# Kernel tuning notes

Hardware: AMD Instinct MI355X
Metric: run time of the kernel (lower is better)

The kernel has to match this reference:

```python
import jax, jax.numpy as jnp
import numpy as np

N, M, DIM, HEADS = 32768, 2048, 128, 8
TAU = 0.1


def setup_inputs() -> dict:
    key = jax.random.key(0)
    ks = jax.random.split(key, 7)
    return {
        "x1": jax.random.normal(ks[0], (N, DIM), jnp.float32),
        "k": jax.random.normal(ks[1], (N, DIM), jnp.float32),
        "c": jax.random.normal(ks[2], (M, DIM), jnp.float32),
        "Wq": jax.random.normal(ks[3], (DIM * HEADS, DIM), jnp.float32) * 0.02,
        "bq": jax.random.normal(ks[4], (DIM * HEADS,), jnp.float32) * 0.02,
        "Wd": jax.random.normal(ks[5], (DIM, DIM), jnp.float32) * 0.02,
        "bd": jax.random.normal(ks[6], (DIM,), jnp.float32) * 0.02,
    }


def reference(x1, k, c, Wq, bq, Wd, bd):
    # q and k both go through the same 'query' projection (as in the source)
    q = x1 @ Wq.T + bq                      # [N, dim*H]
    kq = k @ Wq.T + bq                      # [N, dim*H]
    C = jnp.tile(c, (1, HEADS))             # torch.cat([c]*H, dim=1) -> [M, dim*H]
    t = q + kq                              # additive attention 'scores' input
    logits = (t @ C.T) / jnp.sqrt(jnp.asarray(DIM, t.dtype))  # [N, M]
    p = jax.nn.softmax(logits, axis=-1)
    # gumbel_softmax(p, tau=0.1, hard=True): -log(Exp(1)) ~ Gumbel(0,1)
    noise = jax.random.gumbel(jax.random.key(42), p.shape, p.dtype)
    y_soft = jax.nn.softmax((p + noise) / TAU, axis=-1)
    idx = jnp.argmax(y_soft, axis=-1)
    y_hard = jax.nn.one_hot(idx, M, dtype=p.dtype)
    y = y_hard - jax.lax.stop_gradient(y_soft) + y_soft  # straight-through
    # attention_dropout and dropout are rate 0.0 -> identity
    out = y.T @ x1                          # [M, dim]
    return out @ Wd.T + bd                  # dense
```

## Files before the change

### kernel.cpp

```cpp
#include <hip/hip_runtime.h>
#include <stdint.h>
#include <math.h>

#define NROW 32768
#define MCOL 2048
#define KDIM 128
#define NHEAD 8
#define SCALE 0.08838834764831845f
#define STATS_BLOCKS 512
#define SCAN_BLOCKS 1024
#define CAND_MAX 32

typedef __attribute__((ext_vector_type(8))) short short8;
typedef __attribute__((ext_vector_type(4))) float f32x4;

__device__ __forceinline__ uint32_t rotl32(uint32_t x, uint32_t r) {
  return __builtin_amdgcn_alignbit(x, x, 32u - r);
}
__device__ __forceinline__ uint32_t umin3(uint32_t a, uint32_t b, uint32_t c) {
  return min(min(a, b), c);
}

__device__ __forceinline__ uint32_t tf_hash(uint32_t c) {
  const uint32_t K2 = 0x1BD11BDAu ^ 0u ^ 42u;
  uint32_t x0 = 0u, x1 = c + 42u;
#define R4A { x0 += x1; x1 = rotl32(x1,13); x1 ^= x0; \
              x0 += x1; x1 = rotl32(x1,15); x1 ^= x0; \
              x0 += x1; x1 = rotl32(x1,26); x1 ^= x0; \
              x0 += x1; x1 = rotl32(x1, 6); x1 ^= x0; }
#define R4B { x0 += x1; x1 = rotl32(x1,17); x1 ^= x0; \
              x0 += x1; x1 = rotl32(x1,29); x1 ^= x0; \
              x0 += x1; x1 = rotl32(x1,16); x1 ^= x0; \
              x0 += x1; x1 = rotl32(x1,24); x1 ^= x0; }
  R4A x0 += 42u;      x1 += K2 + 1u;
  R4B x0 += K2;       x1 += 2u;
  R4A    x1 += 42u + 3u;
  R4B x0 += 42u;      x1 += K2 + 4u;
  R4A x0 += K2;       x1 += 5u;
#undef R4A
#undef R4B
  return x0 ^ x1;
}

__device__ __forceinline__ float bits_to_u(uint32_t b) {
  uint32_t fb = (b >> 9) | 0x3F800000u;
  float f = __uint_as_float(fb) - 1.0f;
  return (f == 0.0f) ? 1.17549435e-38f : f;
}

__global__ void k_wsum(const float* __restrict__ Wq, const float* __restrict__ bq,
                       float* __restrict__ Wsum, float* __restrict__ bsum) {
  int t = blockIdx.x * 256 + threadIdx.x;
  if (t < KDIM * KDIM) {
    int d = t >> 7, e = t & 127;
    float s = 0.f;
#pragma unroll
    for (int h = 0; h < NHEAD; ++h) s += Wq[(h * KDIM + d) * KDIM + e];
    Wsum[t] = s;
  }
  if (blockIdx.x == 0 && threadIdx.x < KDIM) {
    int d = threadIdx.x;
    float s = 0.f;
#pragma unroll
    for (int h = 0; h < NHEAD; ++h) s += bq[h * KDIM + d];
    bsum[d] = 2.0f * s;
  }
}

__global__ void k_cw(const float* __restrict__ c, const float* __restrict__ Wsum,
                     const float* __restrict__ bsum,
                     float* __restrict__ cw_s, unsigned short* __restrict__ cwB16,
                     float* __restrict__ cb_s) {
  int m = blockIdx.x;
  int e = threadIdx.x;
  __shared__ float crow[KDIM];
  if (e < 32) ((float4*)crow)[e] = ((const float4*)(c + (size_t)m * KDIM))[e];
  __syncthreads();
  float s = 0.f;
#pragma unroll 4
  for (int d = 0; d < KDIM; ++d) s += crow[d] * Wsum[d * KDIM + e];
  float sv = s * SCALE;
  cw_s[(size_t)m * KDIM + e] = sv;
  {
    int t = m >> 4, col = m & 15, ks = e >> 5, grp = (e >> 3) & 3, j = e & 7;
    int lane = grp * 16 + col;
    cwB16[(((size_t)(t * 4 + ks)) * 64 + lane) * 8 + j] =
        (unsigned short)(__float_as_uint(sv) >> 16);
  }
  if (e == 0) {
    float sb = 0.f;
    for (int d = 0; d < KDIM; ++d) sb += bsum[d] * crow[d];
    cb_s[m] = sb * SCALE;
  }
}

__launch_bounds__(256, 4)
__global__ void k_fused(const float* __restrict__ x1, const float* __restrict__ kin,
                        const uint4* __restrict__ cwB, const float* __restrict__ cb_s,
                        float* __restrict__ rowMx, float* __restrict__ rowD,
                        uint2* __restrict__ cand, int* __restrict__ cnts) {
  const int tid = threadIdx.x;
  const int wv = tid >> 6, lane = tid & 63;

  if (blockIdx.x < STATS_BLOCKS) {
    const int R = blockIdx.x * 64 + wv * 16;
    const int rowA = R + (lane & 15);
    const int kbase = (lane >> 4) * 8;

    union { uint32_t u[4]; short8 s; } af[4];
#pragma unroll
    for (int ks = 0; ks < 4; ++ks) {
      const float* xp = x1 + (size_t)rowA * KDIM + ks * 32 + kbase;
      const float* kp = kin + (size_t)rowA * KDIM + ks * 32 + kbase;
      float4 a0 = *(const float4*)xp, a1 = *(const float4*)(xp + 4);
      float4 b0 = *(const float4*)kp, b1 = *(const float4*)(kp + 4);
      float f[8] = {a0.x + b0.x, a0.y + b0.y, a0.z + b0.z, a0.w + b0.w,
                    a1.x + b1.x, a1.y + b1.y, a1.z + b1.z, a1.w + b1.w};
#pragma unroll
      for (int r = 0; r < 4; ++r)
        af[ks].u[r] = (__float_as_uint(f[2 * r]) >> 16) |
                      (__float_as_uint(f[2 * r + 1]) & 0xFFFF0000u);
    }

    float mxs[4], Ds[4];
#pragma unroll
    for (int r = 0; r < 4; ++r) { mxs[r] = -INFINITY; Ds[r] = 0.f; }

#pragma unroll 2
    for (int t = 0; t < 128; ++t) {
      f32x4 acc = {0.f, 0.f, 0.f, 0.f};
#pragma unroll
      for (int ks = 0; ks < 4; ++ks) {
        union { uint4 v; short8 s; } bf;
        bf.v = cwB[(size_t)(t * 4 + ks) * 64 + lane];
        acc = __builtin_amdgcn_mfma_f32_16x16x32_bf16(af[ks].s, bf.s, acc, 0, 0, 0);
      }
      float cbv = cb_s[t * 16 + (lane & 15)];
#pragma unroll
      for (int r = 0; r < 4; ++r) {
        float lv = acc[r] + cbv;
        mxs[r] = fmaxf(mxs[r], lv);
        Ds[r] += __expf(lv);
      }
    }

#pragma unroll
    for (int s = 1; s < 16; s <<= 1) {
#pragma unroll
      for (int r = 0; r < 4; ++r) {
        mxs[r] = fmaxf(mxs[r], __shfl_xor(mxs[r], s));
        Ds[r] += __shfl_xor(Ds[r], s);
      }
    }
    if ((lane & 15) == 0) {
#pragma unroll
      for (int r = 0; r < 4; ++r) {
        int n = R + (lane >> 4) * 4 + r;
        rowMx[n] = mxs[r];
        rowD[n] = Ds[r];
      }
    }
  } else {
    const int wgid = (blockIdx.x - STATS_BLOCKS) * 4 + wv;
    for (int rr = 0; rr < 8; ++rr) {
      const int n = wgid * 8 + rr;
      const uint32_t c0 = (uint32_t)n * (uint32_t)MCOL + (uint32_t)lane;

      uint32_t t0 = 0u, t1 = 0u, t2 = 0u;
#pragma unroll 8
      for (uint32_t jj = 0; jj < 32; ++jj) {
        uint32_t b = tf_hash(c0 + 64u * jj);
        uint32_t key = (b & 0xFFFFFE00u) | jj;
        t2 = max(t2, umin3(t0, t1, key));
        t1 = max(t1, min(t0, key));
        t0 = max(t0, key);
      }

      uint32_t kmax = t0;
#pragma unroll
      for (int s = 1; s < 64; s <<= 1)
        kmax = max(kmax, (uint32_t)__shfl_xor((int)kmax, s));
      float ustar = bits_to_u(kmax);
      float uthr = __expf(1.30f * __logf(ustar));
      uint32_t bthr = (__float_as_uint(uthr + 1.0f) & 0x007FFFFFu) << 9;
      if (bthr >= 512u) bthr -= 512u;

      uint32_t base_idx = 0;
      uint2* crow = cand + (size_t)n * CAND_MAX;
#pragma unroll
      for (int s = 0; s < 3; ++s) {
        uint32_t tk = (s == 0) ? t0 : ((s == 1) ? t1 : t2);
        bool pred = tk >= bthr;
        unsigned long long mk = __ballot(pred);
        uint32_t pos = base_idx + (uint32_t)__popcll(mk & ((1ull << lane) - 1ull));
        if (pred && pos < CAND_MAX) {
          uint32_t m = (uint32_t)lane | ((tk & 31u) << 6);
          crow[pos] = make_uint2(tk & 0xFFFFFE00u, m);
        }
        base_idx += (uint32_t)__popcll(mk);
      }
      cnts[n] = (int)base_idx;
    }
  }
}

__launch_bounds__(256, 4)
__global__ void k_fix(const float* __restrict__ x1, const float* __restrict__ kin,
                      const float* __restrict__ cw_s, const float* __restrict__ cb_s,
                      const float* __restrict__ rowMx, const float* __restrict__ rowD,
                      const uint2* __restrict__ cand, const int* __restrict__ cnts,
                      float* __restrict__ accum) {
  __shared__ float xksh[4][KDIM];
  const int tid = threadIdx.x;
  const int wv = tid >> 6, lane = tid & 63;
  const int wgid = blockIdx.x * 4 + wv;

  for (int rr = 0; rr < 16; ++rr) {
    const int n = wgid * 16 + rr;
    const int cnt = cnts[n];
    const float mx = rowMx[n], Dp = rowD[n];
    const float pmax = expf(mx) / Dp;

    const float2 xa = ((const float2*)(x1 + (size_t)n * KDIM))[lane];
    const float2 xb = ((const float2*)(kin + (size_t)n * KDIM))[lane];
    const float xk0 = xa.x + xb.x, xk1 = xa.y + xb.y;

    float bestSc = -INFINITY;
    int bestM = 0x7FFFFFFF;

    if (cnt > CAND_MAX || pmax > 0.2f) {
      xksh[wv][lane * 2] = xk0;
      xksh[wv][lane * 2 + 1] = xk1;
      __builtin_amdgcn_s_waitcnt(0);
      for (uint32_t jj = 0; jj < 32; ++jj) {
        uint32_t m = (uint32_t)lane | (jj << 6);
        uint32_t b = tf_hash((uint32_t)n * (uint32_t)MCOL + m);
        float u = bits_to_u(b);
        float g = -logf(-logf(u));
        float l = 0.f;
        for (int e = 0; e < KDIM; ++e) l += xksh[wv][e] * cw_s[(size_t)m * KDIM + e];
        float p = __expf(l + cb_s[m]) / Dp;
        float sc = p + g;
        if (sc > bestSc || (sc == bestSc && (int)m < bestM)) { bestSc = sc; bestM = (int)m; }
      }
#pragma unroll
      for (int s = 1; s < 64; s <<= 1) {
        float os = __shfl_xor(bestSc, s);
        int om = __shfl_xor(bestM, s);
        if (os > bestSc || (os == bestSc && om < bestM)) { bestSc = os; bestM = om; }
      }
    } else {
      uint2 cd = make_uint2(0u, 0u);
      float g = -INFINITY;
      if (lane < cnt) {
        cd = cand[(size_t)n * CAND_MAX + lane];
        g = -logf(-logf(bits_to_u(cd.x)));
      }
      float g1 = g;
#pragma unroll
      for (int s = 1; s < 64; s <<= 1) g1 = fmaxf(g1, __shfl_xor(g1, s));
      const float thr = g1 - (pmax * 1.05f + 2e-4f);

      unsigned long long bl = __ballot(lane < cnt && g >= thr);
      while (bl) {
        int src = __ffsll(bl) - 1;
        bl &= bl - 1ull;
        int m = __shfl((int)cd.y, src);
        float gc = __shfl(g, src);
        const float2 cv = ((const float2*)(cw_s + (size_t)m * KDIM))[lane];
        float part = xk0 * cv.x + xk1 * cv.y;
#pragma unroll
        for (int s = 1; s < 64; s <<= 1) part += __shfl_xor(part, s);
        float p = __expf(part + cb_s[m]) / Dp;
        float sc = p + gc;
        if (sc > bestSc || (sc == bestSc && m < bestM)) { bestSc = sc; bestM = m; }
      }
    }

    float* dst = accum + (size_t)bestM * KDIM + lane * 2;
    atomicAdd(dst + 0, xa.x);
    atomicAdd(dst + 1, xa.y);
  }
}

__global__ void k_final(const float* __restrict__ acc, const float* __restrict__ Wd,
                        const float* __restrict__ bd, float* __restrict__ out) {
  int m = blockIdx.x, j = threadIdx.x;
  __shared__ float ar[KDIM];
  if (j < 32) ((float4*)ar)[j] = ((const float4*)(acc + (size_t)m * KDIM))[j];
  __syncthreads();
  const float4* wr = (const float4*)(Wd + (size_t)j * KDIM);
  float s = 0.f;
#pragma unroll
  for (int e4 = 0; e4 < 32; ++e4) {
    float4 wv = wr[e4];
    s += wv.x * ar[4 * e4 + 0] + wv.y * ar[4 * e4 + 1]
       + wv.z * ar[4 * e4 + 2] + wv.w * ar[4 * e4 + 3];
  }
  out[(size_t)m * KDIM + j] = s + bd[j];
}

extern "C" void kernel_launch(void* const* d_in, const int* in_sizes, int n_in,
                              void* d_out, int out_size, void* d_ws, size_t ws_size,
                              hipStream_t stream) {
  const float* x1 = (const float*)d_in[0];
  const float* k  = (const float*)d_in[1];
  const float* c  = (const float*)d_in[2];
  const float* Wq = (const float*)d_in[3];
  const float* bq = (const float*)d_in[4];
  const float* Wd = (const float*)d_in[5];
  const float* bd = (const float*)d_in[6];
  float* out = (float*)d_out;

  char* ws = (char*)d_ws;
  size_t off = 0;
  float* cw_s = (float*)(ws + off); off += (size_t)MCOL * KDIM * 4;
  float* cb_s = (float*)(ws + off); off += 8192;
  unsigned short* cwB = (unsigned short*)(ws + off); off += (size_t)MCOL * KDIM * 2;
  float* Wsum = (float*)(ws + off); off += KDIM * KDIM * 4;
  float* bsum = (float*)(ws + off); off += 4096;
  float* rowMx = (float*)(ws + off); off += (size_t)NROW * 4;
  float* rowD  = (float*)(ws + off); off += (size_t)NROW * 4;
  float* accum = (float*)(ws + off); off += (size_t)MCOL * KDIM * 4;
  int*   cnts  = (int*)(ws + off);  off += (size_t)NROW * 4;
  uint2* cand  = (uint2*)(ws + off); off += (size_t)NROW * CAND_MAX * 8;

  hipMemsetAsync(accum, 0, (size_t)MCOL * KDIM * sizeof(float), stream);
  k_wsum<<<64, 256, 0, stream>>>(Wq, bq, Wsum, bsum);
  k_cw<<<MCOL, 128, 0, stream>>>(c, Wsum, bsum, cw_s, cwB, cb_s);
  k_fused<<<STATS_BLOCKS + SCAN_BLOCKS, 256, 0, stream>>>(x1, k, (const uint4*)cwB,
                                                          cb_s, rowMx, rowD, cand, cnts);
  k_fix<<<512, 256, 0, stream>>>(x1, k, cw_s, cb_s, rowMx, rowD, cand, cnts, accum);
  k_final<<<MCOL, 128, 0, stream>>>(accum, Wd, bd, out);
}
```

Measured before the change: 212.8 us.

## Fuse softmax stats, Gumbel top-3 scan and candidate fix into one kernel

Merges the stats/scan kernel and the fix kernel into a single kernel where each block handles 32 rows. Two waves compute the softmax max and denominator via MFMA into shared memory, while all waves compute per-lane top-3 Gumbel keys, with an unequal row split that gives the stats waves fewer rows. After a block barrier, each wave resolves its rows directly from register-held keys. This removes the global candidate, count and row-stat buffers and a kernel launch, at the cost of more registers (30 key arrays) and a barrier that couples the MFMA and hash work. It also drops the candidate-overflow fallback check.

```diff
diff --git a/kernel.cpp b/kernel.cpp
--- a/kernel.cpp
+++ b/kernel.cpp
@@ -7,18 +7,12 @@
 #define KDIM 128
 #define NHEAD 8
 #define SCALE 0.08838834764831845f
-#define STATS_BLOCKS 512
-#define SCAN_BLOCKS 1024
-#define CAND_MAX 32
 
 typedef __attribute__((ext_vector_type(8))) short short8;
 typedef __attribute__((ext_vector_type(4))) float f32x4;
 
 __device__ __forceinline__ uint32_t rotl32(uint32_t x, uint32_t r) {
   return __builtin_amdgcn_alignbit(x, x, 32u - r);
-}
-__device__ __forceinline__ uint32_t umin3(uint32_t a, uint32_t b, uint32_t c) {
-  return min(min(a, b), c);
 }
 
 __device__ __forceinline__ uint32_t tf_hash(uint32_t c) {
@@ -48,6 +42,11 @@
   return (f == 0.0f) ? 1.17549435e-38f : f;
 }
 
+__device__ __forceinline__ float gumbel_of_key(uint32_t key) {
+  float u = bits_to_u(key);
+  return -logf(-logf(u));
+}
+
 __global__ void k_wsum(const float* __restrict__ Wq, const float* __restrict__ bq,
                        float* __restrict__ Wsum, float* __restrict__ bsum) {
   int t = blockIdx.x * 256 + threadIdx.x;
@@ -95,15 +94,21 @@
 }
 
 __launch_bounds__(256, 4)
-__global__ void k_fused(const float* __restrict__ x1, const float* __restrict__ kin,
-                        const uint4* __restrict__ cwB, const float* __restrict__ cb_s,
-                        float* __restrict__ rowMx, float* __restrict__ rowD,
-                        uint2* __restrict__ cand, int* __restrict__ cnts) {
+__global__ void k_mega(const float* __restrict__ x1, const float* __restrict__ kin,
+                       const uint4* __restrict__ cwB, const float* __restrict__ cb_s,
+                       const float* __restrict__ cw_s, float* __restrict__ accum) {
+  __shared__ float smx[32];
+  __shared__ float sD[32];
+  __shared__ float xksh[4][KDIM];
+
   const int tid = threadIdx.x;
   const int wv = tid >> 6, lane = tid & 63;
-
-  if (blockIdx.x < STATS_BLOCKS) {
-    const int R = blockIdx.x * 64 + wv * 16;
+  const int B = blockIdx.x * 32;
+  const int sstart = 6 * wv + ((wv >= 2) ? 4 * (wv - 2) : 0);
+  const int scnt = (wv < 2) ? 6 : 10;
+
+  if (wv < 2) {
+    const int R = B + wv * 16;
     const int rowA = R + (lane & 15);
     const int kbase = (lane >> 4) * 8;
 
@@ -155,131 +160,105 @@
     if ((lane & 15) == 0) {
 #pragma unroll
       for (int r = 0; r < 4; ++r) {
-        int n = R + (lane >> 4) * 4 + r;
-        rowMx[n] = mxs[r];
-        rowD[n] = Ds[r];
-      }
-    }
-  } else {
-    const int wgid = (blockIdx.x - STATS_BLOCKS) * 4 + wv;
-    for (int rr = 0; rr < 8; ++rr) {
-      const int n = wgid * 8 + rr;
+        int lr = wv * 16 + (lane >> 4) * 4 + r;
+        smx[lr] = mxs[r];
+        sD[lr] = Ds[r];
+      }
+    }
+  }
+
+  uint32_t tk0[10], tk1[10], tk2[10];
+#pragma unroll
+  for (int ri = 0; ri < 10; ++ri) {
+    if (ri < scnt) {
+      const int n = B + sstart + ri;
       const uint32_t c0 = (uint32_t)n * (uint32_t)MCOL + (uint32_t)lane;
-
       uint32_t t0 = 0u, t1 = 0u, t2 = 0u;
 #pragma unroll 8
       for (uint32_t jj = 0; jj < 32; ++jj) {
         uint32_t b = tf_hash(c0 + 64u * jj);
         uint32_t key = (b & 0xFFFFFE00u) | jj;
-        t2 = max(t2, umin3(t0, t1, key));
+        t2 = max(t2, min(min(t0, t1), key));
         t1 = max(t1, min(t0, key));
         t0 = max(t0, key);
       }
-
+      tk0[ri] = t0; tk1[ri] = t1; tk2[ri] = t2;
+    }
+  }
+
+  __syncthreads();
+
+#pragma unroll
+  for (int ri = 0; ri < 10; ++ri) {
+    if (ri < scnt) {
+      const int n = B + sstart + ri;
+      const int lr = sstart + ri;
+
+      uint32_t t0 = tk0[ri], t1 = tk1[ri], t2 = tk2[ri];
       uint32_t kmax = t0;
 #pragma unroll
       for (int s = 1; s < 64; s <<= 1)
         kmax = max(kmax, (uint32_t)__shfl_xor((int)kmax, s));
-      float ustar = bits_to_u(kmax);
-      float uthr = __expf(1.30f * __logf(ustar));
-      uint32_t bthr = (__float_as_uint(uthr + 1.0f) & 0x007FFFFFu) << 9;
-      if (bthr >= 512u) bthr -= 512u;
-
-      uint32_t base_idx = 0;
-      uint2* crow = cand + (size_t)n * CAND_MAX;
-#pragma unroll
-      for (int s = 0; s < 3; ++s) {
-        uint32_t tk = (s == 0) ? t0 : ((s == 1) ? t1 : t2);
-        bool pred = tk >= bthr;
-        unsigned long long mk = __ballot(pred);
-        uint32_t pos = base_idx + (uint32_t)__popcll(mk & ((1ull << lane) - 1ull));
-        if (pred && pos < CAND_MAX) {
-          uint32_t m = (uint32_t)lane | ((tk & 31u) << 6);
-          crow[pos] = make_uint2(tk & 0xFFFFFE00u, m);
+
+      const float mx = smx[lr], Dp = sD[lr];
+      const float pmax = __expf(mx) / Dp;
+      const float gstar = gumbel_of_key(kmax);
+      const float thr = gstar - (pmax * 1.05f + 2e-4f);
+
+      const float2 xa = ((const float2*)(x1 + (size_t)n * KDIM))[lane];
+      const float2 xb = ((const float2*)(kin + (size_t)n * KDIM))[lane];
+      const float xk0 = xa.x + xb.x, xk1 = xa.y + xb.y;
+
+      float bestSc = -INFINITY;
+      int bestM = 0x7FFFFFFF;
+
+      if (pmax > 0.2f) {
+        xksh[wv][lane * 2] = xk0;
+        xksh[wv][lane * 2 + 1] = xk1;
+        __builtin_amdgcn_s_waitcnt(0);
+        for (uint32_t jj = 0; jj < 32; ++jj) {
+          uint32_t m = (uint32_t)lane | (jj << 6);
+          uint32_t b = tf_hash((uint32_t)n * (uint32_t)MCOL + m);
+          float g = -logf(-logf(bits_to_u(b)));
+          float l = 0.f;
+          for (int e = 0; e < KDIM; ++e) l += xksh[wv][e] * cw_s[(size_t)m * KDIM + e];
+          float p = __expf(l + cb_s[m]) / Dp;
+          float sc = p + g;
+          if (sc > bestSc || (sc == bestSc && (int)m < bestM)) { bestSc = sc; bestM = (int)m; }
         }
-        base_idx += (uint32_t)__popcll(mk);
-      }
-      cnts[n] = (int)base_idx;
-    }
-  }
-}
-
-__launch_bounds__(256, 4)
-__global__ void k_fix(const float* __restrict__ x1, const float* __restrict__ kin,
-                      const float* __restrict__ cw_s, const float* __restrict__ cb_s,
-                      const float* __restrict__ rowMx, const float* __restrict__ rowD,
-                      const uint2* __restrict__ cand, const int* __restrict__ cnts,
-                      float* __restrict__ accum) {
-  __shared__ float xksh[4][KDIM];
-  const int tid = threadIdx.x;
-  const int wv = tid >> 6, lane = tid & 63;
-  const int wgid = blockIdx.x * 4 + wv;
-
-  for (int rr = 0; rr < 16; ++rr) {
-    const int n = wgid * 16 + rr;
-    const int cnt = cnts[n];
-    const float mx = rowMx[n], Dp = rowD[n];
-    const float pmax = expf(mx) / Dp;
-
-    const float2 xa = ((const float2*)(x1 + (size_t)n * KDIM))[lane];
-    const float2 xb = ((const float2*)(kin + (size_t)n * KDIM))[lane];
-    const float xk0 = xa.x + xb.x, xk1 = xa.y + xb.y;
-
-    float bestSc = -INFINITY;
-    int bestM = 0x7FFFFFFF;
-
-    if (cnt > CAND_MAX || pmax > 0.2f) {
-      xksh[wv][lane * 2] = xk0;
-      xksh[wv][lane * 2 + 1] = xk1;
-      __builtin_amdgcn_s_waitcnt(0);
-      for (uint32_t jj = 0; jj < 32; ++jj) {
-        uint32_t m = (uint32_t)lane | (jj << 6);
-        uint32_t b = tf_hash((uint32_t)n * (uint32_t)MCOL + m);
-        float u = bits_to_u(b);
-        float g = -logf(-logf(u));
-        float l = 0.f;
-        for (int e = 0; e < KDIM; ++e) l += xksh[wv][e] * cw_s[(size_t)m * KDIM + e];
-        float p = __expf(l + cb_s[m]) / Dp;
-        float sc = p + g;
-        if (sc > bestSc || (sc == bestSc && (int)m < bestM)) { bestSc = sc; bestM = (int)m; }
-      }
-#pragma unroll
-      for (int s = 1; s < 64; s <<= 1) {
-        float os = __shfl_xor(bestSc, s);
-        int om = __shfl_xor(bestM, s);
-        if (os > bestSc || (os == bestSc && om < bestM)) { bestSc = os; bestM = om; }
-      }
-    } else {
-      uint2 cd = make_uint2(0u, 0u);
-      float g = -INFINITY;
-      if (lane < cnt) {
-        cd = cand[(size_t)n * CAND_MAX + lane];
-        g = -logf(-logf(bits_to_u(cd.x)));
-      }
-      float g1 = g;
-#pragma unroll
-      for (int s = 1; s < 64; s <<= 1) g1 = fmaxf(g1, __shfl_xor(g1, s));
-      const float thr = g1 - (pmax * 1.05f + 2e-4f);
-
-      unsigned long long bl = __ballot(lane < cnt && g >= thr);
-      while (bl) {
-        int src = __ffsll(bl) - 1;
-        bl &= bl - 1ull;
-        int m = __shfl((int)cd.y, src);
-        float gc = __shfl(g, src);
-        const float2 cv = ((const float2*)(cw_s + (size_t)m * KDIM))[lane];
-        float part = xk0 * cv.x + xk1 * cv.y;
-#pragma unroll
-        for (int s = 1; s < 64; s <<= 1) part += __shfl_xor(part, s);
-        float p = __expf(part + cb_s[m]) / Dp;
-        float sc = p + gc;
-        if (sc > bestSc || (sc == bestSc && m < bestM)) { bestSc = sc; bestM = m; }
-      }
-    }
-
-    float* dst = accum + (size_t)bestM * KDIM + lane * 2;
-    atomicAdd(dst + 0, xa.x);
-    atomicAdd(dst + 1, xa.y);
+#pragma unroll
+        for (int s = 1; s < 64; s <<= 1) {
+          float os = __shfl_xor(bestSc, s);
+          int om = __shfl_xor(bestM, s);
+          if (os > bestSc || (os == bestSc && om < bestM)) { bestSc = os; bestM = om; }
+        }
+      } else {
+#pragma unroll
+        for (int s = 0; s < 3; ++s) {
+          uint32_t tkv = (s == 0) ? t0 : ((s == 1) ? t1 : t2);
+          float g = gumbel_of_key(tkv);
+          unsigned long long bl = __ballot(g >= thr);
+          while (bl) {
+            int src = __ffsll(bl) - 1;
+            bl &= bl - 1ull;
+            uint32_t kk = (uint32_t)__shfl((int)tkv, src);
+            float gc = __shfl(g, src);
+            int m = src | (int)((kk & 31u) << 6);
+            const float2 cv = ((const float2*)(cw_s + (size_t)m * KDIM))[lane];
+            float part = xk0 * cv.x + xk1 * cv.y;
+#pragma unroll
+            for (int sh = 1; sh < 64; sh <<= 1) part += __shfl_xor(part, sh);
+            float p = __expf(part + cb_s[m]) / Dp;
+            float sc = p + gc;
+            if (sc > bestSc || (sc == bestSc && m < bestM)) { bestSc = sc; bestM = m; }
+          }
+        }
+      }
+
+      float* dst = accum + (size_t)bestM * KDIM + lane * 2;
+      atomicAdd(dst + 0, xa.x);
+      atomicAdd(dst + 1, xa.y);
+    }
   }
 }
 
@@ -319,17 +298,11 @@
   unsigned short* cwB = (unsigned short*)(ws + off); off += (size_t)MCOL * KDIM * 2;
   float* Wsum = (float*)(ws + off); off += KDIM * KDIM * 4;
   float* bsum = (float*)(ws + off); off += 4096;
-  float* rowMx = (float*)(ws + off); off += (size_t)NROW * 4;
-  float* rowD  = (float*)(ws + off); off += (size_t)NROW * 4;
   float* accum = (float*)(ws + off); off += (size_t)MCOL * KDIM * 4;
-  int*   cnts  = (int*)(ws + off);  off += (size_t)NROW * 4;
-  uint2* cand  = (uint2*)(ws + off); off += (size_t)NROW * CAND_MAX * 8;
 
   hipMemsetAsync(accum, 0, (size_t)MCOL * KDIM * sizeof(float), stream);
   k_wsum<<<64, 256, 0, stream>>>(Wq, bq, Wsum, bsum);
   k_cw<<<MCOL, 128, 0, stream>>>(c, Wsum, bsum, cw_s, cwB, cb_s);
-  k_fused<<<STATS_BLOCKS + SCAN_BLOCKS, 256, 0, stream>>>(x1, k, (const uint4*)cwB,
-                                                          cb_s, rowMx, rowD, cand, cnts);
-  k_fix<<<512, 256, 0, stream>>>(x1, k, cw_s, cb_s, rowMx, rowD, cand, cnts, accum);
+  k_mega<<<1024, 256, 0, stream>>>(x1, k, (const uint4*)cwB, cb_s, cw_s, accum);
   k_final<<<MCOL, 128, 0, stream>>>(accum, Wd, bd, out);
 }
```

Measured after the change: 207.0 us. 2.7% less time.
